# Performance work log

Hardware: AMD Instinct MI355X
Metric: run time of the kernel (lower is better)

The kernel has to match this reference:

```python
import jax, jax.numpy as jnp
import numpy as np

N_SUBJECTS = 16
N_LABELS = 8
DENS_TEMP = 0.1  # args.ProtoSim_dens_temp


def setup_inputs() -> dict:
    key = jax.random.key(0)
    k1, k2, k3 = jax.random.split(key, 3)
    B, V, D = 131072, 2, 128
    X_data = jax.random.normal(k1, (B, V, D), dtype=jnp.float32)
    subject = jax.random.randint(k2, (B,), 0, N_SUBJECTS, dtype=jnp.int64) if jax.config.read('jax_enable_x64') else jax.random.randint(k2, (B,), 0, N_SUBJECTS)
    labels = jax.random.randint(k3, (B,), 0, N_LABELS)
    return {"X_data": X_data, "subject": subject, "labels": labels}


def reference(X_data, subject, labels):
    B, V, D = X_data.shape
    G = N_SUBJECTS * N_LABELS
    # torch.cat(torch.unbind(X_data, dim=1), dim=0): view-major ordering -> [V*B, D]
    cf = jnp.transpose(X_data, (1, 0, 2)).reshape(V * B, D)
    # subject/labels duplicated once (module assumes 2 views)
    seg = jnp.tile(subject * N_LABELS + labels, V)  # group id per row, [V*B]
    counts = jax.ops.segment_sum(jnp.ones((V * B,), jnp.float32), seg, num_segments=G)
    centroid = jax.ops.segment_sum(cf, seg, num_segments=G) / counts[:, None]  # [G, D]
    # per-point euclidean distance to own group centroid (torch.cdist to 1-row centroid)
    dist = jnp.linalg.norm(cf - centroid[seg], axis=1)  # [V*B]
    # density: mean(sqrt(dist)) / log(n + 10) for groups with n > 1, else 0 then dmax
    dens = (jax.ops.segment_sum(jnp.sqrt(dist), seg, num_segments=G) / counts) / jnp.log(counts + 10.0)
    dens = jnp.where(counts > 1, dens, 0.0)
    dens = jnp.where(counts > 1, dens, dens.max())
    lo = jnp.percentile(dens, 10.0)
    hi = jnp.percentile(dens, 90.0)
    dens = jnp.clip(dens, lo, hi)
    dens = DENS_TEMP * dens / dens.mean()
    cen_of_cen = centroid.mean(axis=0)  # [D]
    sim = jnp.exp((centroid @ cen_of_cen) / dens)  # [G]
    sim = sim - sim.max()
    return -sim.mean()
```

## Files before the change

kernel.cpp:

```cpp
#include <hip/hip_runtime.h>
#include <cstdint>
#include <cstddef>

#define BPTS    131072
#define D_DIM   128
#define G_GR    128
#define NL      8
#define GD      (G_GR * D_DIM)
#define NBLK    256
#define TPB     1024
#define PPB     (BPTS / NBLK)
#define GPW     (G_GR / (TPB / 64))

__device__ __forceinline__ float dpp_add(float d, const int ctrl) {
    int s;
    switch (ctrl) {
    case 0x111: s = __builtin_amdgcn_update_dpp(0, __float_as_int(d), 0x111, 0xf, 0xf, true); break;
    case 0x112: s = __builtin_amdgcn_update_dpp(0, __float_as_int(d), 0x112, 0xf, 0xf, true); break;
    case 0x114: s = __builtin_amdgcn_update_dpp(0, __float_as_int(d), 0x114, 0xf, 0xf, true); break;
    case 0x118: s = __builtin_amdgcn_update_dpp(0, __float_as_int(d), 0x118, 0xf, 0xf, true); break;
    case 0x142: s = __builtin_amdgcn_update_dpp(0, __float_as_int(d), 0x142, 0xf, 0xf, true); break;
    default:    s = __builtin_amdgcn_update_dpp(0, __float_as_int(d), 0x143, 0xf, 0xf, true); break;
    }
    return d + __int_as_float(s);
}

__device__ __forceinline__ float sum64(float d) {
    d = dpp_add(d, 0x111);
    d = dpp_add(d, 0x112);
    d = dpp_add(d, 0x114);
    d = dpp_add(d, 0x118);
    d = dpp_add(d, 0x142);
    d = dpp_add(d, 0x143);
    return d;
}

__global__ __launch_bounds__(TPB) void k_centroid(const float* __restrict__ Xf,
                                                  const int* __restrict__ sub,
                                                  const int* __restrict__ lab,
                                                  float* __restrict__ cpart,
                                                  int* __restrict__ hpart,
                                                  int* __restrict__ goffG,
                                                  int* __restrict__ glistG) {
    __shared__ int glist[PPB];
    __shared__ int goff[G_GR];
    __shared__ int hist[G_GR];
    __shared__ int cursor[G_GR];
    __shared__ int scan[G_GR];
    int t = threadIdx.x, blk = blockIdx.x;
    int lane = t & 63, w = t >> 6;
    int pbase = blk * PPB;

    if (t < G_GR) hist[t] = 0;
    __syncthreads();
    int myg = -1;
    if (t < PPB) {
        myg = sub[pbase + t] * NL + lab[pbase + t];
        atomicAdd(&hist[myg], 1);
    }
    __syncthreads();
    if (t < G_GR) scan[t] = hist[t];
    __syncthreads();
    for (int s = 1; s < G_GR; s <<= 1) {
        int v = 0;
        if (t < G_GR) { v = scan[t]; if (t >= s) v += scan[t - s]; }
        __syncthreads();
        if (t < G_GR) scan[t] = v;
        __syncthreads();
    }
    if (t < G_GR) { goff[t] = scan[t] - hist[t]; cursor[t] = scan[t] - hist[t]; }
    __syncthreads();
    if (t < PPB) {
        int pos = atomicAdd(&cursor[myg], 1);
        glist[pos] = t;
    }
    __syncthreads();

    if (t < G_GR) {
        hpart[blk * G_GR + t] = hist[t];
        goffG[blk * G_GR + t] = goff[t];
    }
    if (t < PPB) glistG[blk * PPB + t] = glist[t];

    for (int gi = 0; gi < GPW; ++gi) {
        int g = w * GPW + gi;
        int s = goff[g], n = hist[g];
        float ax = 0.f, ay = 0.f;
        int k = 0;
        for (; k + 4 <= n; k += 4) {
            int p0 = pbase + glist[s + k + 0];
            int p1 = pbase + glist[s + k + 1];
            int p2 = pbase + glist[s + k + 2];
            int p3 = pbase + glist[s + k + 3];
            const float* r0 = Xf + (size_t)p0 * 256;
            const float* r1 = Xf + (size_t)p1 * 256;
            const float* r2 = Xf + (size_t)p2 * 256;
            const float* r3 = Xf + (size_t)p3 * 256;
            float2 a0 = *(const float2*)(r0 + 2 * lane);
            float2 b0 = *(const float2*)(r0 + 128 + 2 * lane);
            float2 a1 = *(const float2*)(r1 + 2 * lane);
            float2 b1 = *(const float2*)(r1 + 128 + 2 * lane);
            float2 a2 = *(const float2*)(r2 + 2 * lane);
            float2 b2 = *(const float2*)(r2 + 128 + 2 * lane);
            float2 a3 = *(const float2*)(r3 + 2 * lane);
            float2 b3 = *(const float2*)(r3 + 128 + 2 * lane);
            ax += (a0.x + b0.x) + (a1.x + b1.x) + (a2.x + b2.x) + (a3.x + b3.x);
            ay += (a0.y + b0.y) + (a1.y + b1.y) + (a2.y + b2.y) + (a3.y + b3.y);
        }
        for (; k < n; ++k) {
            int p = pbase + glist[s + k];
            const float* r = Xf + (size_t)p * 256;
            float2 a = *(const float2*)(r + 2 * lane);
            float2 b = *(const float2*)(r + 128 + 2 * lane);
            ax += a.x + b.x;
            ay += a.y + b.y;
        }
        float2 o; o.x = ax; o.y = ay;
        *(float2*)(cpart + (size_t)blk * GD + (size_t)g * D_DIM + 2 * lane) = o;
    }
}

__global__ __launch_bounds__(512) void k_reduce(const float* __restrict__ cpart,
                                                const int* __restrict__ hpart,
                                                float* __restrict__ centroid,
                                                float* __restrict__ countsf) {
    __shared__ float red[8][64];
    __shared__ int   hred[64];
    __shared__ float cf2s;
    int g = blockIdx.x >> 1, h = blockIdx.x & 1;
    int t = threadIdx.x;
    int dl = t & 63, bs = t >> 6;
    int d = h * 64 + dl;

    float a0 = 0.f, a1 = 0.f, a2 = 0.f, a3 = 0.f;
    for (int b = bs; b < NBLK; b += 32) {
        a0 += cpart[(size_t)(b)      * GD + g * D_DIM + d];
        a1 += cpart[(size_t)(b + 8)  * GD + g * D_DIM + d];
        a2 += cpart[(size_t)(b + 16) * GD + g * D_DIM + d];
        a3 += cpart[(size_t)(b + 24) * GD + g * D_DIM + d];
    }
    red[bs][dl] = (a0 + a1) + (a2 + a3);

    if (t < 64) {
        int hacc = 0;
        for (int b = t; b < NBLK; b += 64) hacc += hpart[b * G_GR + g];
        hred[t] = hacc;
    }
    __syncthreads();
    if (t == 0) {
        int n = 0;
        for (int i = 0; i < 64; ++i) n += hred[i];
        cf2s = 2.f * (float)n;
        if (h == 0) countsf[g] = cf2s;
    }
    __syncthreads();
    if (t < 64) {
        float v = 0.f;
#pragma unroll
        for (int r = 0; r < 8; ++r) v += red[r][t];
        float cf2 = cf2s;
        centroid[g * D_DIM + h * 64 + t] = (cf2 > 0.f) ? v / cf2 : 0.f;
    }
}

__global__ __launch_bounds__(TPB) void k_distn(const float* __restrict__ Xf,
                                               const int* __restrict__ hpart,
                                               const int* __restrict__ goffG,
                                               const int* __restrict__ glistG,
                                               const float* __restrict__ centroid,
                                               float* __restrict__ dpart) {
    __shared__ int glist[PPB];
    __shared__ int goff[G_GR];
    __shared__ int hist[G_GR];
    int t = threadIdx.x, blk = blockIdx.x;
    int lane = t & 63, w = t >> 6;
    int pbase = blk * PPB;

    if (t < G_GR) {
        hist[t] = hpart[blk * G_GR + t];
        goff[t] = goffG[blk * G_GR + t];
    }
    if (t < PPB) glist[t] = glistG[blk * PPB + t];
    __syncthreads();

    for (int gi = 0; gi < GPW; ++gi) {
        int g = w * GPW + gi;
        int s = goff[g], n = hist[g];
        float2 c = *(const float2*)(centroid + (size_t)g * D_DIM + 2 * lane);
        float sacc = 0.f;
        int k = 0;
        for (; k + 2 <= n; k += 2) {
            int p0 = pbase + glist[s + k];
            int p1 = pbase + glist[s + k + 1];
            const float* r0 = Xf + (size_t)p0 * 256;
            const float* r1 = Xf + (size_t)p1 * 256;
            float2 a0 = *(const float2*)(r0 + 2 * lane);
            float2 b0 = *(const float2*)(r0 + 128 + 2 * lane);
            float2 a1 = *(const float2*)(r1 + 2 * lane);
            float2 b1 = *(const float2*)(r1 + 128 + 2 * lane);
            float e0 = a0.x - c.x, e1 = a0.y - c.y;
            float f0 = b0.x - c.x, f1 = b0.y - c.y;
            float g0 = a1.x - c.x, g1 = a1.y - c.y;
            float h0 = b1.x - c.x, h1 = b1.y - c.y;
            float d0 = sum64(e0 * e0 + e1 * e1);
            float d1 = sum64(f0 * f0 + f1 * f1);
            float d2 = sum64(g0 * g0 + g1 * g1);
            float d3 = sum64(h0 * h0 + h1 * h1);
            sacc += (sqrtf(sqrtf(d0)) + sqrtf(sqrtf(d1)))
                  + (sqrtf(sqrtf(d2)) + sqrtf(sqrtf(d3)));
        }
        if (k < n) {
            int p = pbase + glist[s + k];
            const float* r = Xf + (size_t)p * 256;
            float2 a = *(const float2*)(r + 2 * lane);
            float2 b = *(const float2*)(r + 128 + 2 * lane);
            float e0 = a.x - c.x, e1 = a.y - c.y;
            float f0 = b.x - c.x, f1 = b.y - c.y;
            float d0 = sum64(e0 * e0 + e1 * e1);
            float d1 = sum64(f0 * f0 + f1 * f1);
            sacc += sqrtf(sqrtf(d0)) + sqrtf(sqrtf(d1));
        }
        if (lane == 63) dpart[blk * G_GR + g] = sacc;
    }
}

__global__ __launch_bounds__(512) void k_final(const float* __restrict__ dpart,
                                               const float* __restrict__ countsf,
                                               const float* __restrict__ centroid,
                                               float* __restrict__ out) {
    __shared__ float sl4[4][G_GR];
    __shared__ float srt[G_GR];
    __shared__ float red[G_GR];
    __shared__ float cocs[D_DIM];
    __shared__ float dotv[G_GR];
    __shared__ float densv[G_GR];
    int t = threadIdx.x;
    int col = t & 127, q = t >> 7;
    int lane = t & 63, w8 = t >> 6;

    float a0 = 0.f, a1 = 0.f;
    for (int b = q; b < NBLK; b += 8) {
        a0 += dpart[(b)     * G_GR + col];
        a1 += dpart[(b + 4) * G_GR + col];
    }
    sl4[q][col] = a0 + a1;
    __syncthreads();

    float dens = 0.f, cnt = 0.f;
    if (t < G_GR) {
        float ds = sl4[0][t] + sl4[1][t] + sl4[2][t] + sl4[3][t];
        cnt = countsf[t];
        dens = (cnt > 1.f) ? (ds / cnt) / logf(cnt + 10.f) : 0.f;
        red[t] = dens;
    }
    __syncthreads();
    for (int s = 64; s > 0; s >>= 1) {
        if (t < s) red[t] = fmaxf(red[t], red[t + s]);
        __syncthreads();
    }
    float dmax = red[0];
    __syncthreads();
    if (t < G_GR && !(cnt > 1.f)) dens = dmax;

    if (t < G_GR) srt[t] = dens;
    __syncthreads();
    for (int k = 2; k <= G_GR; k <<= 1) {
        for (int j = k >> 1; j > 0; j >>= 1) {
            int ixj = t ^ j;
            if (t < G_GR && ixj > t) {
                float a = srt[t], b = srt[ixj];
                bool up = ((t & k) == 0);
                if ((a > b) == up) { srt[t] = b; srt[ixj] = a; }
            }
            __syncthreads();
        }
    }
    double p10 = 0.10 * 127.0, p90 = 0.90 * 127.0;
    int   i10 = (int)p10,           i90 = (int)p90;
    float f10 = (float)(p10 - i10), f90 = (float)(p90 - i90);
    float lo = srt[i10] + f10 * (srt[i10 + 1] - srt[i10]);
    float hi = srt[i90] + f90 * (srt[i90 + 1] - srt[i90]);
    if (t < G_GR) dens = fminf(fmaxf(dens, lo), hi);

    if (t < G_GR) red[t] = dens;
    __syncthreads();
    for (int s = 64; s > 0; s >>= 1) {
        if (t < s) red[t] += red[t + s];
        __syncthreads();
    }
    float dmean = red[0] / 128.f;
    __syncthreads();
    if (t < G_GR) densv[t] = 0.1f * dens / dmean;

    float cs = 0.f;
    for (int g = q; g < G_GR; g += 4) cs += centroid[g * D_DIM + col];
    sl4[q][col] = cs;
    __syncthreads();
    if (t < D_DIM)
        cocs[t] = (sl4[0][t] + sl4[1][t] + sl4[2][t] + sl4[3][t]) / 128.f;
    __syncthreads();

    {
        float2 co = *(const float2*)&cocs[2 * lane];
        for (int i = 0; i < 16; ++i) {
            int g = w8 * 16 + i;
            float2 c = *(const float2*)(centroid + (size_t)g * D_DIM + 2 * lane);
            float p = c.x * co.x + c.y * co.y;
            float s = sum64(p);
            if (lane == 63) dotv[g] = s;
        }
    }
    __syncthreads();

    float sim = 0.f;
    if (t < G_GR) {
        sim = expf(dotv[t] / densv[t]);
        red[t] = sim;
    }
    __syncthreads();
    for (int s = 64; s > 0; s >>= 1) {
        if (t < s) red[t] = fmaxf(red[t], red[t + s]);
        __syncthreads();
    }
    float smax = red[0];
    __syncthreads();
    if (t < G_GR) red[t] = sim - smax;
    __syncthreads();
    for (int s = 64; s > 0; s >>= 1) {
        if (t < s) red[t] += red[t + s];
        __syncthreads();
    }
    if (t == 0) out[0] = -(red[0] / 128.f);
}

extern "C" void kernel_launch(void* const* d_in, const int* in_sizes, int n_in,
                              void* d_out, int out_size, void* d_ws, size_t ws_size,
                              hipStream_t stream) {
    const float*  Xf      = (const float*)d_in[0];
    const int*    subject = (const int*)d_in[1];
    const int*    labels  = (const int*)d_in[2];
    float*        out     = (float*)d_out;
    char*         ws      = (char*)d_ws;

    size_t o = 0;
    float* cpart    = (float*)(ws + o); o += (size_t)NBLK * GD * 4;
    int*   hpart    = (int*)(ws + o);   o += (size_t)NBLK * G_GR * 4;
    int*   goffG    = (int*)(ws + o);   o += (size_t)NBLK * G_GR * 4;
    int*   glistG   = (int*)(ws + o);   o += (size_t)NBLK * PPB * 4;
    float* centroid = (float*)(ws + o); o += (size_t)GD * 4;
    float* countsf  = (float*)(ws + o); o += 512;
    float* dpart    = (float*)(ws + o); o += (size_t)NBLK * G_GR * 4;

    k_centroid<<<NBLK, TPB, 0, stream>>>(Xf, subject, labels, cpart, hpart, goffG, glistG);
    k_reduce  <<<G_GR * 2, 512, 0, stream>>>(cpart, hpart, centroid, countsf);
    k_distn   <<<NBLK, TPB, 0, stream>>>(Xf, hpart, goffG, glistG, centroid, dpart);
    k_final   <<<1, 512, 0, stream>>>(dpart, countsf, centroid, out);
}
```

Before: 264.8 us.

## Fuse four kernels into one cooperative kernel with grid-wide syncs

Merges the centroid, reduce, distance and final kernels into a single cooperative launch separated by grid.sync barriers. Each block keeps its per-block group list in shared memory, so the global glist/goff spill and reload are gone. The final density and dot-product work is spread across 128 blocks before one block finishes. This removes three kernel launch gaps and the re-staging traffic, at the cost of grid-barrier overhead and needing all 256 blocks of 1024 threads to be co-resident.

```diff
diff --git a/kernel.cpp b/kernel.cpp
--- a/kernel.cpp
+++ b/kernel.cpp
@@ -1,6 +1,9 @@
 #include <hip/hip_runtime.h>
+#include <hip/hip_cooperative_groups.h>
 #include <cstdint>
 #include <cstddef>
+
+namespace cg = cooperative_groups;
 
 #define BPTS    131072
 #define D_DIM   128
@@ -35,18 +38,27 @@
     return d;
 }
 
-__global__ __launch_bounds__(TPB) void k_centroid(const float* __restrict__ Xf,
-                                                  const int* __restrict__ sub,
-                                                  const int* __restrict__ lab,
-                                                  float* __restrict__ cpart,
-                                                  int* __restrict__ hpart,
-                                                  int* __restrict__ goffG,
-                                                  int* __restrict__ glistG) {
-    __shared__ int glist[PPB];
-    __shared__ int goff[G_GR];
-    __shared__ int hist[G_GR];
-    __shared__ int cursor[G_GR];
-    __shared__ int scan[G_GR];
+__global__ __launch_bounds__(TPB) void k_all(const float* __restrict__ Xf,
+                                             const int* __restrict__ sub,
+                                             const int* __restrict__ lab,
+                                             float* __restrict__ cpart,
+                                             int* __restrict__ hpart,
+                                             float* __restrict__ centroid,
+                                             float* __restrict__ countsf,
+                                             float* __restrict__ cocG,
+                                             float* __restrict__ dpart,
+                                             float* __restrict__ densp,
+                                             float* __restrict__ dotv,
+                                             float* __restrict__ out) {
+    cg::grid_group grid = cg::this_grid();
+    __shared__ int   glist[PPB];
+    __shared__ int   goff[G_GR];
+    __shared__ int   hist[G_GR];
+    __shared__ int   cursor[G_GR];
+    __shared__ int   scan[G_GR];
+    __shared__ float fred[TPB];
+    __shared__ float cf2s;
+
     int t = threadIdx.x, blk = blockIdx.x;
     int lane = t & 63, w = t >> 6;
     int pbase = blk * PPB;
@@ -75,12 +87,7 @@
         glist[pos] = t;
     }
     __syncthreads();
-
-    if (t < G_GR) {
-        hpart[blk * G_GR + t] = hist[t];
-        goffG[blk * G_GR + t] = goff[t];
-    }
-    if (t < PPB) glistG[blk * PPB + t] = glist[t];
+    if (t < G_GR) hpart[blk * G_GR + t] = hist[t];
 
     for (int gi = 0; gi < GPW; ++gi) {
         int g = w * GPW + gi;
@@ -118,70 +125,41 @@
         float2 o; o.x = ax; o.y = ay;
         *(float2*)(cpart + (size_t)blk * GD + (size_t)g * D_DIM + 2 * lane) = o;
     }
-}
-
-__global__ __launch_bounds__(512) void k_reduce(const float* __restrict__ cpart,
-                                                const int* __restrict__ hpart,
-                                                float* __restrict__ centroid,
-                                                float* __restrict__ countsf) {
-    __shared__ float red[8][64];
-    __shared__ int   hred[64];
-    __shared__ float cf2s;
-    int g = blockIdx.x >> 1, h = blockIdx.x & 1;
-    int t = threadIdx.x;
-    int dl = t & 63, bs = t >> 6;
-    int d = h * 64 + dl;
-
-    float a0 = 0.f, a1 = 0.f, a2 = 0.f, a3 = 0.f;
-    for (int b = bs; b < NBLK; b += 32) {
-        a0 += cpart[(size_t)(b)      * GD + g * D_DIM + d];
-        a1 += cpart[(size_t)(b + 8)  * GD + g * D_DIM + d];
-        a2 += cpart[(size_t)(b + 16) * GD + g * D_DIM + d];
-        a3 += cpart[(size_t)(b + 24) * GD + g * D_DIM + d];
-    }
-    red[bs][dl] = (a0 + a1) + (a2 + a3);
-
-    if (t < 64) {
-        int hacc = 0;
-        for (int b = t; b < NBLK; b += 64) hacc += hpart[b * G_GR + g];
-        hred[t] = hacc;
-    }
-    __syncthreads();
-    if (t == 0) {
-        int n = 0;
-        for (int i = 0; i < 64; ++i) n += hred[i];
-        cf2s = 2.f * (float)n;
-        if (h == 0) countsf[g] = cf2s;
-    }
-    __syncthreads();
-    if (t < 64) {
-        float v = 0.f;
+    grid.sync();
+
+    {
+        int g = blk >> 1, h = blk & 1;
+        int dl = t & 63, bs = t >> 6;
+        int d = h * 64 + dl;
+        float a0 = 0.f, a1 = 0.f, a2 = 0.f, a3 = 0.f;
+        for (int b = bs; b < NBLK; b += 64) {
+            a0 += cpart[(size_t)(b)      * GD + g * D_DIM + d];
+            a1 += cpart[(size_t)(b + 16) * GD + g * D_DIM + d];
+            a2 += cpart[(size_t)(b + 32) * GD + g * D_DIM + d];
+            a3 += cpart[(size_t)(b + 48) * GD + g * D_DIM + d];
+        }
+        fred[t] = (a0 + a1) + (a2 + a3);
+        if (t < G_GR) {
+            int hacc = hpart[t * G_GR + g] + hpart[(t + 128) * G_GR + g];
+            scan[t] = hacc;
+        }
+        __syncthreads();
+        if (t == 0) {
+            int n = 0;
+            for (int i = 0; i < G_GR; ++i) n += scan[i];
+            cf2s = 2.f * (float)n;
+            if (h == 0) countsf[g] = cf2s;
+        }
+        __syncthreads();
+        if (t < 64) {
+            float v = 0.f;
 #pragma unroll
-        for (int r = 0; r < 8; ++r) v += red[r][t];
-        float cf2 = cf2s;
-        centroid[g * D_DIM + h * 64 + t] = (cf2 > 0.f) ? v / cf2 : 0.f;
-    }
-}
-
-__global__ __launch_bounds__(TPB) void k_distn(const float* __restrict__ Xf,
-                                               const int* __restrict__ hpart,
-                                               const int* __restrict__ goffG,
-                                               const int* __restrict__ glistG,
-                                               const float* __restrict__ centroid,
-                                               float* __restrict__ dpart) {
-    __shared__ int glist[PPB];
-    __shared__ int goff[G_GR];
-    __shared__ int hist[G_GR];
-    int t = threadIdx.x, blk = blockIdx.x;
-    int lane = t & 63, w = t >> 6;
-    int pbase = blk * PPB;
-
-    if (t < G_GR) {
-        hist[t] = hpart[blk * G_GR + t];
-        goff[t] = goffG[blk * G_GR + t];
-    }
-    if (t < PPB) glist[t] = glistG[blk * PPB + t];
-    __syncthreads();
+            for (int r = 0; r < 16; ++r) v += fred[r * 64 + t];
+            float cf2 = cf2s;
+            centroid[g * D_DIM + h * 64 + t] = (cf2 > 0.f) ? v / cf2 : 0.f;
+        }
+    }
+    grid.sync();
 
     for (int gi = 0; gi < GPW; ++gi) {
         int g = w * GPW + gi;
@@ -220,117 +198,113 @@
             float d1 = sum64(f0 * f0 + f1 * f1);
             sacc += sqrtf(sqrtf(d0)) + sqrtf(sqrtf(d1));
         }
-        if (lane == 63) dpart[blk * G_GR + g] = sacc;
-    }
-}
-
-__global__ __launch_bounds__(512) void k_final(const float* __restrict__ dpart,
-                                               const float* __restrict__ countsf,
-                                               const float* __restrict__ centroid,
-                                               float* __restrict__ out) {
-    __shared__ float sl4[4][G_GR];
-    __shared__ float srt[G_GR];
-    __shared__ float red[G_GR];
-    __shared__ float cocs[D_DIM];
-    __shared__ float dotv[G_GR];
-    __shared__ float densv[G_GR];
-    int t = threadIdx.x;
-    int col = t & 127, q = t >> 7;
-    int lane = t & 63, w8 = t >> 6;
-
-    float a0 = 0.f, a1 = 0.f;
-    for (int b = q; b < NBLK; b += 8) {
-        a0 += dpart[(b)     * G_GR + col];
-        a1 += dpart[(b + 4) * G_GR + col];
-    }
-    sl4[q][col] = a0 + a1;
-    __syncthreads();
-
-    float dens = 0.f, cnt = 0.f;
-    if (t < G_GR) {
-        float ds = sl4[0][t] + sl4[1][t] + sl4[2][t] + sl4[3][t];
-        cnt = countsf[t];
-        dens = (cnt > 1.f) ? (ds / cnt) / logf(cnt + 10.f) : 0.f;
-        red[t] = dens;
-    }
-    __syncthreads();
-    for (int s = 64; s > 0; s >>= 1) {
-        if (t < s) red[t] = fmaxf(red[t], red[t + s]);
-        __syncthreads();
-    }
-    float dmax = red[0];
-    __syncthreads();
-    if (t < G_GR && !(cnt > 1.f)) dens = dmax;
-
-    if (t < G_GR) srt[t] = dens;
-    __syncthreads();
-    for (int k = 2; k <= G_GR; k <<= 1) {
-        for (int j = k >> 1; j > 0; j >>= 1) {
-            int ixj = t ^ j;
-            if (t < G_GR && ixj > t) {
-                float a = srt[t], b = srt[ixj];
-                bool up = ((t & k) == 0);
-                if ((a > b) == up) { srt[t] = b; srt[ixj] = a; }
+        if (lane == 63) dpart[(size_t)g * NBLK + blk] = sacc;
+    }
+    if (blk == 0) {
+        int col = t & 127, q = t >> 7;
+        float cs = 0.f;
+        for (int g = q; g < G_GR; g += 8) cs += centroid[g * D_DIM + col];
+        __syncthreads();
+        fred[q * 128 + col] = cs;
+        __syncthreads();
+        if (t < D_DIM) {
+            float v = 0.f;
+#pragma unroll
+            for (int r = 0; r < 8; ++r) v += fred[r * 128 + t];
+            cocG[t] = v / 128.f;
+        }
+    }
+    grid.sync();
+
+    if (blk < G_GR) {
+        int g = blk;
+        fred[t] = (t < NBLK) ? dpart[(size_t)g * NBLK + t] : 0.f;
+        __syncthreads();
+        for (int s = 512; s > 0; s >>= 1) {
+            if (t < s) fred[t] += fred[t + s];
+            __syncthreads();
+        }
+        float dsum = fred[0];
+        float cnt = countsf[g];
+        if (t == 0)
+            densp[g] = (cnt > 1.f) ? (dsum / cnt) / logf(cnt + 10.f) : 0.f;
+        __syncthreads();
+        fred[t] = (t < D_DIM) ? centroid[(size_t)g * D_DIM + t] * cocG[t] : 0.f;
+        __syncthreads();
+        for (int s = 512; s > 0; s >>= 1) {
+            if (t < s) fred[t] += fred[t + s];
+            __syncthreads();
+        }
+        if (t == 0) dotv[g] = fred[0];
+    }
+    grid.sync();
+
+    if (blk == 0) {
+        float* srt = fred;
+        float* red = fred + 128;
+        float dens = 0.f, cnt = 0.f;
+        if (t < G_GR) {
+            cnt = countsf[t];
+            dens = densp[t];
+            red[t] = dens;
+        }
+        __syncthreads();
+        for (int s = 64; s > 0; s >>= 1) {
+            if (t < s) red[t] = fmaxf(red[t], red[t + s]);
+            __syncthreads();
+        }
+        float dmax = red[0];
+        __syncthreads();
+        if (t < G_GR && !(cnt > 1.f)) dens = dmax;
+        if (t < G_GR) srt[t] = dens;
+        __syncthreads();
+        for (int k = 2; k <= G_GR; k <<= 1) {
+            for (int j = k >> 1; j > 0; j >>= 1) {
+                int ixj = t ^ j;
+                if (t < G_GR && ixj > t) {
+                    float a = srt[t], b = srt[ixj];
+                    bool up = ((t & k) == 0);
+                    if ((a > b) == up) { srt[t] = b; srt[ixj] = a; }
+                }
+                __syncthreads();
             }
-            __syncthreads();
-        }
-    }
-    double p10 = 0.10 * 127.0, p90 = 0.90 * 127.0;
-    int   i10 = (int)p10,           i90 = (int)p90;
-    float f10 = (float)(p10 - i10), f90 = (float)(p90 - i90);
-    float lo = srt[i10] + f10 * (srt[i10 + 1] - srt[i10]);
-    float hi = srt[i90] + f90 * (srt[i90 + 1] - srt[i90]);
-    if (t < G_GR) dens = fminf(fmaxf(dens, lo), hi);
-
-    if (t < G_GR) red[t] = dens;
-    __syncthreads();
-    for (int s = 64; s > 0; s >>= 1) {
-        if (t < s) red[t] += red[t + s];
-        __syncthreads();
-    }
-    float dmean = red[0] / 128.f;
-    __syncthreads();
-    if (t < G_GR) densv[t] = 0.1f * dens / dmean;
-
-    float cs = 0.f;
-    for (int g = q; g < G_GR; g += 4) cs += centroid[g * D_DIM + col];
-    sl4[q][col] = cs;
-    __syncthreads();
-    if (t < D_DIM)
-        cocs[t] = (sl4[0][t] + sl4[1][t] + sl4[2][t] + sl4[3][t]) / 128.f;
-    __syncthreads();
-
-    {
-        float2 co = *(const float2*)&cocs[2 * lane];
-        for (int i = 0; i < 16; ++i) {
-            int g = w8 * 16 + i;
-            float2 c = *(const float2*)(centroid + (size_t)g * D_DIM + 2 * lane);
-            float p = c.x * co.x + c.y * co.y;
-            float s = sum64(p);
-            if (lane == 63) dotv[g] = s;
-        }
-    }
-    __syncthreads();
-
-    float sim = 0.f;
-    if (t < G_GR) {
-        sim = expf(dotv[t] / densv[t]);
-        red[t] = sim;
-    }
-    __syncthreads();
-    for (int s = 64; s > 0; s >>= 1) {
-        if (t < s) red[t] = fmaxf(red[t], red[t + s]);
-        __syncthreads();
-    }
-    float smax = red[0];
-    __syncthreads();
-    if (t < G_GR) red[t] = sim - smax;
-    __syncthreads();
-    for (int s = 64; s > 0; s >>= 1) {
-        if (t < s) red[t] += red[t + s];
-        __syncthreads();
-    }
-    if (t == 0) out[0] = -(red[0] / 128.f);
+        }
+        double p10 = 0.10 * 127.0, p90 = 0.90 * 127.0;
+        int   i10 = (int)p10,           i90 = (int)p90;
+        float f10 = (float)(p10 - i10), f90 = (float)(p90 - i90);
+        float lo = srt[i10] + f10 * (srt[i10 + 1] - srt[i10]);
+        float hi = srt[i90] + f90 * (srt[i90 + 1] - srt[i90]);
+        if (t < G_GR) dens = fminf(fmaxf(dens, lo), hi);
+        __syncthreads();
+        if (t < G_GR) red[t] = dens;
+        __syncthreads();
+        for (int s = 64; s > 0; s >>= 1) {
+            if (t < s) red[t] += red[t + s];
+            __syncthreads();
+        }
+        float dmean = red[0] / 128.f;
+        __syncthreads();
+        float sim = 0.f;
+        if (t < G_GR) {
+            float dv = 0.1f * dens / dmean;
+            sim = expf(dotv[t] / dv);
+            red[t] = sim;
+        }
+        __syncthreads();
+        for (int s = 64; s > 0; s >>= 1) {
+            if (t < s) red[t] = fmaxf(red[t], red[t + s]);
+            __syncthreads();
+        }
+        float smax = red[0];
+        __syncthreads();
+        if (t < G_GR) red[t] = sim - smax;
+        __syncthreads();
+        for (int s = 64; s > 0; s >>= 1) {
+            if (t < s) red[t] += red[t + s];
+            __syncthreads();
+        }
+        if (t == 0) out[0] = -(red[0] / 128.f);
+    }
 }
 
 extern "C" void kernel_launch(void* const* d_in, const int* in_sizes, int n_in,
@@ -345,14 +319,16 @@
     size_t o = 0;
     float* cpart    = (float*)(ws + o); o += (size_t)NBLK * GD * 4;
     int*   hpart    = (int*)(ws + o);   o += (size_t)NBLK * G_GR * 4;
-    int*   goffG    = (int*)(ws + o);   o += (size_t)NBLK * G_GR * 4;
-    int*   glistG   = (int*)(ws + o);   o += (size_t)NBLK * PPB * 4;
     float* centroid = (float*)(ws + o); o += (size_t)GD * 4;
     float* countsf  = (float*)(ws + o); o += 512;
-    float* dpart    = (float*)(ws + o); o += (size_t)NBLK * G_GR * 4;
-
-    k_centroid<<<NBLK, TPB, 0, stream>>>(Xf, subject, labels, cpart, hpart, goffG, glistG);
-    k_reduce  <<<G_GR * 2, 512, 0, stream>>>(cpart, hpart, centroid, countsf);
-    k_distn   <<<NBLK, TPB, 0, stream>>>(Xf, hpart, goffG, glistG, centroid, dpart);
-    k_final   <<<1, 512, 0, stream>>>(dpart, countsf, centroid, out);
+    float* cocG     = (float*)(ws + o); o += 512;
+    float* dpart    = (float*)(ws + o); o += (size_t)G_GR * NBLK * 4;
+    float* densp    = (float*)(ws + o); o += 512;
+    float* dotv     = (float*)(ws + o); o += 512;
+
+    void* args[] = {(void*)&Xf, (void*)&subject, (void*)&labels, (void*)&cpart,
+                    (void*)&hpart, (void*)&centroid, (void*)&countsf, (void*)&cocG,
+                    (void*)&dpart, (void*)&densp, (void*)&dotv, (void*)&out};
+    hipLaunchCooperativeKernel((const void*)k_all, dim3(NBLK), dim3(TPB),
+                               args, 0, stream);
 }
```

Result: slower. 364.9 us (+37.8%).
